# Kernel optimization log

Hardware: AMD Instinct MI355X
Metric: run time of the kernel (lower is better)

## Reference

```python
import jax, jax.numpy as jnp
import numpy as np

N = 8192
IN_DIM = 512
MEM_DIM = 512


def _linear_params(k, fan_in, fan_out):
    kw, kb = jax.random.split(k)
    s = 1.0 / np.sqrt(fan_in)
    W = jax.random.uniform(kw, (fan_in, fan_out), jnp.float32, -s, s)
    b = jax.random.uniform(kb, (fan_out,), jnp.float32, -s, s)
    return W, b


def setup_inputs() -> dict:
    key = jax.random.key(0)
    ks = jax.random.split(key, 12)
    inputs = jax.random.normal(ks[0], (N, IN_DIM), jnp.float32)
    # tree.type is a [1,2] mixing matrix per node (lang vs vis weights)
    type_mask = jax.nn.softmax(jax.random.normal(ks[1], (N, 2), jnp.float32), axis=-1)
    # topologically ordered tree: parent slot of node i is in [0, i]; slot 0 = virtual zero root state
    rng = np.random.default_rng(0)
    parent = np.zeros(N, dtype=np.int32)
    for i in range(1, N):
        parent[i] = rng.integers(0, i + 1)
    d = {"inputs": inputs, "type_mask": type_mask, "parent": jnp.asarray(parent)}
    names = ["ioux_vis", "iouh_vis", "fx_vis", "fh_vis",
             "ioux_lang", "iouh_lang", "fx_lang", "fh_lang"]
    fanins = [IN_DIM, MEM_DIM, IN_DIM, MEM_DIM] * 2
    fanouts = [3 * MEM_DIM, 3 * MEM_DIM, MEM_DIM, MEM_DIM] * 2
    for j, nm in enumerate(names):
        W, b = _linear_params(ks[2 + j], fanins[j], fanouts[j])
        d["W_" + nm] = W
        d["b_" + nm] = b
    return d


def reference(inputs, type_mask, parent,
              W_ioux_vis, b_ioux_vis, W_iouh_vis, b_iouh_vis,
              W_fx_vis, b_fx_vis, W_fh_vis, b_fh_vis,
              W_ioux_lang, b_ioux_lang, W_iouh_lang, b_iouh_lang,
              W_fx_lang, b_fx_lang, W_fh_lang, b_fh_lang):
    n_nodes = inputs.shape[0]
    D = W_fh_vis.shape[1]
    # batch the input-dependent projections into big GEMMs (fused across all nodes)
    x_iou_v = inputs @ W_ioux_vis + b_ioux_vis  # [N, 3D]
    x_f_v = inputs @ W_fx_vis + b_fx_vis        # [N, D]
    x_iou_l = inputs @ W_ioux_lang + b_ioux_lang
    x_f_l = inputs @ W_fx_lang + b_fx_lang

    def node(x_iou, x_f, h_p, c_p, W_iouh, b_iouh, W_fh, b_fh):
        iou = x_iou + h_p @ W_iouh + b_iouh  # [3D]
        i, o, u = jnp.split(iou, 3)
        f = jax.nn.sigmoid(x_f + h_p @ W_fh + b_fh)
        c = jax.nn.sigmoid(i) * jnp.tanh(u) + f * c_p
        h = jax.nn.sigmoid(o) * jnp.tanh(c)
        return c, h

    # slot 0 holds the zero state used by root nodes; node i lives at slot i+1
    c0 = jnp.zeros((n_nodes + 1, D), inputs.dtype)
    h0 = jnp.zeros((n_nodes + 1, D), inputs.dtype)

    def step(carry, xs):
        c_all, h_all = carry
        n, p, xiv, xfv, xil, xfl, tm = xs
        h_p = h_all[p]
        c_p = c_all[p]
        c_v, h_v = node(xiv, xfv, h_p, c_p, W_iouh_vis, b_iouh_vis, W_fh_vis, b_fh_vis)
        c_l, h_l = node(xil, xfl, h_p, c_p, W_iouh_lang, b_iouh_lang, W_fh_lang, b_fh_lang)
        # type_mask @ cat([lang, vis]) == tm[0]*lang + tm[1]*vis
        c_n = tm[0] * c_l + tm[1] * c_v
        h_n = tm[0] * h_l + tm[1] * h_v  # dropout is identity in eval
        return (c_all.at[n + 1].set(c_n), h_all.at[n + 1].set(h_n)), None

    idx = jnp.arange(n_nodes)
    (c_all, h_all), _ = jax.lax.scan(
        step, (c0, h0), (idx, parent, x_iou_v, x_f_v, x_iou_l, x_f_l, type_mask))
    return c_all[1:], h_all[1:]
```

## Files before the change

kernel.cpp:

```cpp
#include <hip/hip_runtime.h>
#include <math.h>

typedef unsigned short ushort_t;
typedef unsigned int uint_t;
typedef unsigned long long u64_t;
typedef __attribute__((ext_vector_type(8))) short short8;
typedef __attribute__((ext_vector_type(4))) float f32x4;

#define N_NODES 8192
#define DIM 512
#define KTOT 1024
#define NCOLS 4096
#define BM 128
#define BN 128
#define NTILE (NCOLS / BN)
#define KIT (KTOT / 32)
#define WIMG_USHORTS ((size_t)NTILE * KIT * 4096)
#define MAXLEV_LDS 128

__device__ __forceinline__ float sigm(float x) { return 1.0f / (1.0f + __expf(-x)); }
__device__ __forceinline__ float tanh_fast(float x) {
    float ax = fabsf(x);
    float e = __expf(2.0f * ax);
    float t = 1.0f - 2.0f / (e + 1.0f);
    return copysignf(t, x);
}
__device__ __forceinline__ uint_t packf(float f) {
    uint_t u = __float_as_uint(f);
    uint_t hi = u & 0xffff0000u;
    float r = f - __uint_as_float(hi);
    return hi | (__float_as_uint(r) >> 16);
}
__device__ __forceinline__ float unpackw(uint_t w) {
    return __uint_as_float(w & 0xffff0000u) + __uint_as_float(w << 16);
}
__device__ __forceinline__ uint_t rne16(float f) {
    uint_t u = __float_as_uint(f);
    return (u + 0x7fffu + ((u >> 16) & 1u)) >> 16;
}

__device__ __forceinline__ void fragAB_u32(const uint4 w0, const uint4 w1,
                                           short8& hi8, short8& lo8) {
    union { uint_t w[4]; short8 s; } H, L;
    uint_t u[8] = { w0.x, w0.y, w0.z, w0.w, w1.x, w1.y, w1.z, w1.w };
#pragma unroll
    for (int j = 0; j < 4; ++j) {
        H.w[j] = (u[2 * j + 1] & 0xffff0000u) | (u[2 * j] >> 16);
        L.w[j] = (u[2 * j + 1] << 16) | (u[2 * j] & 0xffffu);
    }
    hi8 = H.s; lo8 = L.s;
}

__device__ __forceinline__ void fragA_f32(const float4 f0, const float4 f1,
                                          short8& hi8, short8& lo8) {
    union { uint_t w[4]; short8 s; } H, L;
    float f[8] = { f0.x, f0.y, f0.z, f0.w, f1.x, f1.y, f1.z, f1.w };
#pragma unroll
    for (int j = 0; j < 4; ++j) {
        float a = f[2 * j], b = f[2 * j + 1];
        uint_t h0 = __float_as_uint(a) & 0xffff0000u;
        uint_t h1 = __float_as_uint(b) & 0xffff0000u;
        float r0 = a - __uint_as_float(h0);
        float r1 = b - __uint_as_float(h1);
        H.w[j] = h1 | (h0 >> 16);
        L.w[j] = (__float_as_uint(r1) & 0xffff0000u) | (__float_as_uint(r0) >> 16);
    }
    hi8 = H.s; lo8 = L.s;
}

__global__ void __launch_bounds__(256) prep_wimg_kernel(
    const float* __restrict__ Wx_iou_v, const float* __restrict__ Wh_iou_v,
    const float* __restrict__ Wx_f_v,   const float* __restrict__ Wh_f_v,
    const float* __restrict__ Wx_iou_l, const float* __restrict__ Wh_iou_l,
    const float* __restrict__ Wx_f_l,   const float* __restrict__ Wh_f_l,
    ushort_t* __restrict__ Wimg)
{
    __shared__ float T[32][132];
    int p = blockIdx.x >> 5, it = blockIdx.x & 31;
    int tid = threadIdx.x;
#pragma unroll
    for (int e = 0; e < 16; ++e) {
        int lin = e * 256 + tid;
        int dloc = lin & 15, kk = (lin >> 4) & 31, q = lin >> 9;
        int d = p * 16 + dloc;
        int qq = q & 3; bool lang = q >= 4;
        int k = it * 32 + kk;
        const float* W; int col, stride;
        if (qq < 3) { col = qq * DIM + d; stride = 3 * DIM;
            W = (k < DIM) ? (lang ? Wx_iou_l : Wx_iou_v) : (lang ? Wh_iou_l : Wh_iou_v); }
        else        { col = d; stride = DIM;
            W = (k < DIM) ? (lang ? Wx_f_l : Wx_f_v) : (lang ? Wh_f_l : Wh_f_v); }
        int kr = (k < DIM) ? k : (k - DIM);
        T[kk][dloc * 8 + q] = W[(size_t)kr * stride + col];
    }
    __syncthreads();
    size_t tilebase = (size_t)blockIdx.x * 4096;
#pragma unroll
    for (int gch = 0; gch < 2; ++gch) {
        int gi = gch * 256 + tid;
        int col = gi >> 2, gd = gi & 3;
        uint_t wds[4];
#pragma unroll
        for (int i = 0; i < 4; ++i) {
            uint_t v0 = rne16(T[gd * 8 + 2 * i][col]);
            uint_t v1 = rne16(T[gd * 8 + 2 * i + 1][col]);
            wds[i] = (v1 << 16) | v0;
        }
        *(uint4*)(Wimg + tilebase + (size_t)gi * 8) = make_uint4(wds[0], wds[1], wds[2], wds[3]);
    }
}

__global__ void prep_bias_kernel(
    const float* __restrict__ bx_iou_v, const float* __restrict__ bh_iou_v,
    const float* __restrict__ bx_f_v,   const float* __restrict__ bh_f_v,
    const float* __restrict__ bx_iou_l, const float* __restrict__ bh_iou_l,
    const float* __restrict__ bx_f_l,   const float* __restrict__ bh_f_l,
    float* __restrict__ bias)
{
    int j = blockIdx.x * blockDim.x + threadIdx.x;
    if (j >= NCOLS) return;
    int d = j >> 3, q = j & 7;
    int qq = q & 3;
    bool lang = (q & 4) != 0;
    const float* bx; const float* bh; int col;
    if (qq < 3) { col = qq * DIM + d; bx = lang ? bx_iou_l : bx_iou_v; bh = lang ? bh_iou_l : bh_iou_v; }
    else        { col = d;            bx = lang ? bx_f_l  : bx_f_v;   bh = lang ? bh_f_l  : bh_f_v; }
    bias[j] = bx[col] + bh[col];
}

__global__ void __launch_bounds__(1024) levels_sort_kernel(
    const int* __restrict__ parent,
    int* __restrict__ order, int* __restrict__ offsets,
    int* __restrict__ counts, int* __restrict__ cursors,
    int* __restrict__ nlev, int* __restrict__ tilestart,
    int* __restrict__ rbStart, int* __restrict__ nodeHrb)
{
    __shared__ int s_level[N_NODES];
    __shared__ int s_assigned;
    __shared__ int s_maxlev;
    int tid = threadIdx.x;
    int pr[8];
#pragma unroll
    for (int ii = 0; ii < 8; ++ii) {
        int i = tid + ii * 1024;
        pr[ii] = parent[i];
        s_level[i] = -1;
    }
    for (int i = tid; i <= N_NODES; i += 1024) counts[i] = 0;
    if (tid == 0) { s_assigned = 0; s_maxlev = 0; }
    __syncthreads();

    for (int pass = 0; pass <= N_NODES; ++pass) {
        int newly = 0;
#pragma unroll
        for (int ii = 0; ii < 8; ++ii) {
            int i = tid + ii * 1024;
            if (s_level[i] < 0) {
                int p = pr[ii];
                if (p == 0) { s_level[i] = 0; newly++; }
                else { int lp = s_level[p - 1]; if (lp >= 0) { s_level[i] = lp + 1; newly++; } }
            }
        }
        if (newly) atomicAdd(&s_assigned, newly);
        __syncthreads();
        int a = s_assigned;
        if (a >= N_NODES) break;
        __syncthreads();
    }

#pragma unroll
    for (int ii = 0; ii < 8; ++ii) {
        int i = tid + ii * 1024;
        int lv = s_level[i];
        atomicAdd(&counts[lv], 1);
        atomicMax(&s_maxlev, lv);
    }
    __syncthreads();
    if (tid == 0) {
        int nl = s_maxlev + 1;
        nlev[0] = nl;
        int off = 0, toff = 0, rb = 0;
        for (int l = 0; l < nl; ++l) {
            offsets[l] = off; cursors[l] = off;
            tilestart[l] = toff; rbStart[l] = rb;
            int mt = (counts[l] + BM - 1) / BM;
            rb += mt;
            toff += mt * NTILE;
            off += counts[l];
        }
        offsets[nl] = off;
        tilestart[nl] = toff;
        rbStart[nl] = rb;
        nlev[1] = toff;
    }
    __syncthreads();
#pragma unroll
    for (int ii = 0; ii < 8; ++ii) {
        int i = tid + ii * 1024;
        int lv = s_level[i];
        int pos = atomicAdd(&cursors[lv], 1);
        order[pos] = i;
        nodeHrb[i] = rbStart[lv] + ((pos - offsets[lv]) >> 7);
    }
}

__global__ void __launch_bounds__(256, 2) tree_fused_kernel(
    const float* __restrict__ inputs, const float* __restrict__ type_mask,
    const ushort_t* __restrict__ Wimg, const float* __restrict__ bias,
    const int* __restrict__ order, const int* __restrict__ offsets,
    const int* __restrict__ nlev, const int* __restrict__ parent,
    const int* __restrict__ rbStart,
    int* __restrict__ colCnt,
    uint_t* __restrict__ hPack, uint_t* __restrict__ cPack,
    float* __restrict__ out)
{
    float* cOut = out;
    float* hOut = out + (size_t)N_NODES * DIM;

    __shared__ float eps[BM * 132];
    __shared__ int s_node[BM];
    __shared__ int s_par[BM];
    __shared__ float s_tm[BM][2];
    __shared__ int s_rbs[MAXLEV_LDS];
    __shared__ int s_off[MAXLEV_LDS];
    __shared__ int s_cok[32];
    __shared__ int s_ok[8];

    int tid = threadIdx.x;
    int lane = tid & 63, w = tid >> 6, wr = w >> 1, wc = w & 1;
    int l15 = lane & 15, g = lane >> 4;
    int nl = nlev[0];
    int total = nlev[1];

    int nload = nl + 1; if (nload > MAXLEV_LDS) nload = MAXLEV_LDS;
    for (int i = tid; i < nload; i += 256) { s_rbs[i] = rbStart[i]; s_off[i] = offsets[i]; }
    __syncthreads();

    const ushort_t* bLane = Wimg + (size_t)(wc * 64 + l15) * 32 + (size_t)g * 8;

#define LDB(RB, tilebase, itt) { \
    _Pragma("unroll") for (int n_ = 0; n_ < 4; ++n_) \
        RB[n_] = *(const uint4*)(bLane + (size_t)(tilebase + (itt)) * 4096 + n_ * 512); }

#define LDA_H(RA, itrel) { \
    _Pragma("unroll") for (int m_ = 0; m_ < 4; ++m_) { \
        const uint4* p_ = (const uint4*)(aBaseH[m_] + (itrel) * 32 + g * 8); \
        RA[m_][0] = p_[0]; RA[m_][1] = p_[1]; } }

#define LDA_X(RA, itt) { \
    _Pragma("unroll") for (int m_ = 0; m_ < 4; ++m_) { \
        const float4* p_ = (const float4*)(aBaseX[m_] + (itt) * 32 + g * 8); \
        RA[m_][0] = p_[0]; RA[m_][1] = p_[1]; } }

#define COMP_H(RA, RB) { \
    short8 bh_[4]; \
    _Pragma("unroll") for (int n_ = 0; n_ < 4; ++n_) { \
        union { uint4 u; short8 s; } c_; c_.u = RB[n_]; bh_[n_] = c_.s; } \
    _Pragma("unroll") for (int m_ = 0; m_ < 4; ++m_) { \
        short8 ah_, al_; fragAB_u32(RA[m_][0], RA[m_][1], ah_, al_); \
        _Pragma("unroll") for (int n_ = 0; n_ < 4; ++n_) { \
            acc[m_][n_] = __builtin_amdgcn_mfma_f32_16x16x32_bf16(ah_, bh_[n_], acc[m_][n_], 0, 0, 0); \
            acc[m_][n_] = __builtin_amdgcn_mfma_f32_16x16x32_bf16(al_, bh_[n_], acc[m_][n_], 0, 0, 0); } } }

#define COMP_X(RA, RB) { \
    short8 bh_[4]; \
    _Pragma("unroll") for (int n_ = 0; n_ < 4; ++n_) { \
        union { uint4 u; short8 s; } c_; c_.u = RB[n_]; bh_[n_] = c_.s; } \
    _Pragma("unroll") for (int m_ = 0; m_ < 4; ++m_) { \
        short8 ah_, al_; fragA_f32(RA[m_][0], RA[m_][1], ah_, al_); \
        _Pragma("unroll") for (int n_ = 0; n_ < 4; ++n_) { \
            acc[m_][n_] = __builtin_amdgcn_mfma_f32_16x16x32_bf16(ah_, bh_[n_], acc[m_][n_], 0, 0, 0); \
            acc[m_][n_] = __builtin_amdgcn_mfma_f32_16x16x32_bf16(al_, bh_[n_], acc[m_][n_], 0, 0, 0); } } }

#define WAIT_GROUPS(colPrev, nPrev, gq) { \
    for (;;) { \
        if (tid < 32) \
            s_cok[tid] = (__hip_atomic_load(&(colPrev)[tid], __ATOMIC_RELAXED, \
                                            __HIP_MEMORY_SCOPE_AGENT) >= (nPrev)) ? 1 : 0; \
        __syncthreads(); \
        if (tid < 8) { \
            if (s_cok[4 * tid] && s_cok[4 * tid + 1] && s_cok[4 * tid + 2] && s_cok[4 * tid + 3]) \
                s_ok[tid] = 1; \
        } \
        __syncthreads(); \
        if (s_ok[gq]) break; \
        __builtin_amdgcn_s_sleep(4); \
    } }

    for (int t = blockIdx.x; t < total; t += gridDim.x) {
        int lev = 0;
        while (lev + 1 < nload && s_rbs[lev + 1] * NTILE <= t) ++lev;
        int lt = t - s_rbs[lev] * NTILE;
        int ntile = lt % NTILE;
        int mt = lt / NTILE;
        int start = s_off[lev];
        int cnt = s_off[lev + 1] - start;
        int jc = ntile * BN;
        int r0 = mt * BM;
        int tbx = ntile * KIT;
        int tbh = ntile * KIT + 16;

        if (tid < BM) {
            int r = r0 + tid;
            int node = (r < cnt) ? order[start + r] : -1;
            s_node[tid] = node;
            int p = (node >= 0) ? parent[node] : 0;
            s_par[tid] = p;
            float t0 = 0.f, t1 = 0.f;
            if (node >= 0) { t0 = type_mask[node * 2]; t1 = type_mask[node * 2 + 1]; }
            s_tm[tid][0] = t0; s_tm[tid][1] = t1;
        }
        if (tid < 32) s_cok[tid] = 0;
        if (tid < 8) s_ok[tid] = 0;
        __syncthreads();

        f32x4 acc[4][4];
#pragma unroll
        for (int m = 0; m < 4; ++m)
#pragma unroll
            for (int n = 0; n < 4; ++n) acc[m][n] = (f32x4)(0.f);

        {
            const float* aBaseX[4];
#pragma unroll
            for (int m = 0; m < 4; ++m) {
                int nd = s_node[wr * 64 + m * 16 + l15];
                aBaseX[m] = inputs + (size_t)(nd < 0 ? 0 : nd) * DIM;
            }
            float4 xa0[4][2], xa1[4][2]; uint4 xb0[4], xb1[4];
            LDA_X(xa0, 0); LDB(xb0, tbx, 0);
#pragma unroll
            for (int ii = 0; ii < 8; ++ii) {
                int e = 2 * ii, o = e + 1;
                LDA_X(xa1, o); LDB(xb1, tbx, o);
                __builtin_amdgcn_s_setprio(1);
                COMP_X(xa0, xb0);
                __builtin_amdgcn_s_setprio(0);
                if (e + 2 < 16) { LDA_X(xa0, e + 2); LDB(xb0, tbx, e + 2); }
                __builtin_amdgcn_s_setprio(1);
                COMP_X(xa1, xb1);
                __builtin_amdgcn_s_setprio(0);
            }
        }

        if (lev > 0) {
            const int* colPrev = colCnt + (lev - 1) * NTILE;
            int nPrev = s_rbs[lev] - s_rbs[lev - 1];
            const int gb = ntile >> 2;

            const uint_t* aBaseH[4];
#pragma unroll
            for (int m = 0; m < 4; ++m) {
                int p = s_par[wr * 64 + m * 16 + l15];
                aBaseH[m] = hPack + (size_t)((p > 0) ? (p - 1) : 0) * DIM;
            }

            uint4 ha0[4][2], ha1[4][2]; uint4 hb0[4], hb1[4];
            WAIT_GROUPS(colPrev, nPrev, gb);
            LDA_H(ha0, 2 * gb); LDB(hb0, tbh, 2 * gb);
            LDA_H(ha1, 2 * gb + 1); LDB(hb1, tbh, 2 * gb + 1);
#pragma unroll
            for (int s = 0; s < 8; ++s) {
                const int gn = (gb + s + 1) & 7;
                __builtin_amdgcn_s_setprio(1);
                COMP_H(ha0, hb0);
                __builtin_amdgcn_s_setprio(0);
                if (s < 7) {
                    if (!s_ok[gn]) WAIT_GROUPS(colPrev, nPrev, gn);
                    LDA_H(ha0, 2 * gn); LDB(hb0, tbh, 2 * gn);
                }
                __builtin_amdgcn_s_setprio(1);
                COMP_H(ha1, hb1);
                __builtin_amdgcn_s_setprio(0);
                if (s < 7) { LDA_H(ha1, 2 * gn + 1); LDB(hb1, tbh, 2 * gn + 1); }
            }
        }

        int cntloc = cnt - r0; if (cntloc > BM) cntloc = BM;

        float CP[8];
#pragma unroll
        for (int e = 0; e < 8; ++e) {
            int task = e * 256 + tid;
            int row = task >> 4, dl = task & 15;
            CP[e] = 0.f;
            if (row < cntloc) {
                int p = s_par[row];
                if (p > 0) {
                    int d = (jc + dl * 8) >> 3;
                    CP[e] = unpackw(cPack[(size_t)(p - 1) * DIM + d]);
                }
            }
        }

#pragma unroll
        for (int m = 0; m < 4; ++m)
#pragma unroll
            for (int n = 0; n < 4; ++n) {
                int row = wr * 64 + m * 16 + g * 4;
                int c = wc * 64 + n * 16 + l15;
#pragma unroll
                for (int r = 0; r < 4; ++r) eps[(row + r) * 132 + c] = acc[m][n][r];
            }
        __syncthreads();

        float CN[8], HN[8];
#pragma unroll
        for (int e = 0; e < 8; ++e) {
            int task = e * 256 + tid;
            int row = task >> 4, dl = task & 15;
            CN[e] = 0.f; HN[e] = 0.f;
            if (row < cntloc) {
                int node = s_node[row];
                const float* ep = &eps[row * 132 + dl * 8];
                float4 v0 = *(const float4*)ep;
                float4 v1 = *(const float4*)(ep + 4);
                int jb = jc + dl * 8;
                float4 b0 = *(const float4*)(bias + jb);
                float4 b1 = *(const float4*)(bias + jb + 4);
                float cp = CP[e];
                float cv = sigm(v0.x + b0.x) * tanh_fast(v0.z + b0.z)
                         + sigm(v0.w + b0.w) * cp;
                float hv = sigm(v0.y + b0.y) * tanh_fast(cv);
                float cl = sigm(v1.x + b1.x) * tanh_fast(v1.z + b1.z)
                         + sigm(v1.w + b1.w) * cp;
                float hl = sigm(v1.y + b1.y) * tanh_fast(cl);
                float tm0 = s_tm[row][0], tm1 = s_tm[row][1];
                float cn = tm0 * cl + tm1 * cv;
                float hn2 = tm0 * hl + tm1 * hv;
                CN[e] = cn; HN[e] = hn2;
                size_t oi = (size_t)node * DIM + (jb >> 3);
                __hip_atomic_store(&cPack[oi], packf(cn),
                                   __ATOMIC_RELAXED, __HIP_MEMORY_SCOPE_AGENT);
                __hip_atomic_store(&hPack[oi], packf(hn2),
                                   __ATOMIC_RELAXED, __HIP_MEMORY_SCOPE_AGENT);
            }
        }

        __builtin_amdgcn_s_waitcnt(0);
        __syncthreads();
        if (tid == 0)
            __hip_atomic_fetch_add(&colCnt[lev * NTILE + ntile], 1,
                                   __ATOMIC_RELAXED, __HIP_MEMORY_SCOPE_AGENT);

#pragma unroll
        for (int e = 0; e < 8; ++e) {
            int task = e * 256 + tid;
            int row = task >> 4, dl = task & 15;
            if (row < cntloc) {
                int node = s_node[row];
                size_t oi = (size_t)node * DIM + ((jc + dl * 8) >> 3);
                cOut[oi] = CN[e];
                hOut[oi] = HN[e];
            }
        }
        __syncthreads();
    }
#undef LDB
#undef LDA_H
#undef LDA_X
#undef COMP_H
#undef COMP_X
#undef WAIT_GROUPS
}

extern "C" void kernel_launch(void* const* d_in, const int* in_sizes, int n_in,
                              void* d_out, int out_size, void* d_ws, size_t ws_size,
                              hipStream_t stream) {
    const float* inputs      = (const float*)d_in[0];
    const float* type_mask   = (const float*)d_in[1];
    const int*   parent      = (const int*)d_in[2];
    const float* W_ioux_vis  = (const float*)d_in[3];
    const float* b_ioux_vis  = (const float*)d_in[4];
    const float* W_iouh_vis  = (const float*)d_in[5];
    const float* b_iouh_vis  = (const float*)d_in[6];
    const float* W_fx_vis    = (const float*)d_in[7];
    const float* b_fx_vis    = (const float*)d_in[8];
    const float* W_fh_vis    = (const float*)d_in[9];
    const float* b_fh_vis    = (const float*)d_in[10];
    const float* W_ioux_lang = (const float*)d_in[11];
    const float* b_ioux_lang = (const float*)d_in[12];
    const float* W_iouh_lang = (const float*)d_in[13];
    const float* b_iouh_lang = (const float*)d_in[14];
    const float* W_fx_lang   = (const float*)d_in[15];
    const float* b_fx_lang   = (const float*)d_in[16];
    const float* W_fh_lang   = (const float*)d_in[17];
    const float* b_fh_lang   = (const float*)d_in[18];

    ushort_t* Wimg = (ushort_t*)d_ws;
    float* bias    = (float*)(Wimg + WIMG_USHORTS);
    int* order     = (int*)(bias + NCOLS);
    int* offsets   = order + N_NODES;
    int* counts    = offsets + (N_NODES + 2);
    int* cursors   = counts + (N_NODES + 2);
    int* nlev      = cursors + (N_NODES + 2);
    int* tilestart = nlev + 8;
    int* rbStart   = tilestart + (N_NODES + 2);
    int* nodeHrb   = rbStart + (N_NODES + 2);
    int* colCnt    = nodeHrb + N_NODES;
    size_t off2 = (size_t)((char*)(colCnt + MAXLEV_LDS * NTILE) - (char*)d_ws);
    off2 = (off2 + 255) & ~(size_t)255;
    uint_t* hPack = (uint_t*)((char*)d_ws + off2);
    uint_t* cPack = hPack + (size_t)N_NODES * DIM;

    float* out = (float*)d_out;

    hipMemsetAsync((void*)colCnt, 0, MAXLEV_LDS * NTILE * sizeof(int), stream);

    hipLaunchKernelGGL(prep_wimg_kernel, dim3(NTILE * KIT), dim3(256), 0, stream,
                       W_ioux_vis, W_iouh_vis, W_fx_vis, W_fh_vis,
                       W_ioux_lang, W_iouh_lang, W_fx_lang, W_fh_lang, Wimg);
    hipLaunchKernelGGL(prep_bias_kernel, dim3(NCOLS / 256), dim3(256), 0, stream,
                       b_ioux_vis, b_iouh_vis, b_fx_vis, b_fh_vis,
                       b_ioux_lang, b_iouh_lang, b_fx_lang, b_fh_lang, bias);
    hipLaunchKernelGGL(levels_sort_kernel, dim3(1), dim3(1024), 0, stream,
                       parent, order, offsets, counts, cursors, nlev, tilestart,
                       rbStart, nodeHrb);

    int occ = 0;
    if (hipOccupancyMaxActiveBlocksPerMultiprocessor(&occ, (const void*)tree_fused_kernel, 256, 0) != hipSuccess || occ < 1)
        occ = 1;
    int bpc = occ < 2 ? occ : 2;
    dim3 grid(256 * bpc);

    void* args[] = { (void*)&inputs, (void*)&type_mask, (void*)&Wimg, (void*)&bias,
                     (void*)&order, (void*)&offsets, (void*)&nlev, (void*)&parent,
                     (void*)&rbStart, (void*)&colCnt,
                     (void*)&hPack, (void*)&cPack, (void*)&out };
    hipLaunchCooperativeKernel((const void*)tree_fused_kernel, grid, dim3(256), args, 0, stream);
}
```

Before: 807.8 us.

## Split tree tile across eight waves and gate dependency waits per wave

Doubles the block to 512 threads so each of eight waves computes 32 rows of the 128x128 tile instead of 64, halving per-wave accumulators and A-fragment loads. Replaces the block-wide dependency wait, which used shared flags and two __syncthreads per poll, with a per-wave gate that polls the four column counters itself and tracks satisfied groups in a register mask. It also moves the odd-step prefetch to the end of the loop body. The aim is more latency hiding and less barrier cost on the critical recurrence path. In exchange, the register budget per thread is tighter under the new launch bounds, and more waves poll global counters at once.

```diff
diff --git a/kernel.cpp b/kernel.cpp
--- a/kernel.cpp
+++ b/kernel.cpp
@@ -204,7 +204,7 @@
     }
 }
 
-__global__ void __launch_bounds__(256, 2) tree_fused_kernel(
+__global__ void __launch_bounds__(512, 2) tree_fused_kernel(
     const float* __restrict__ inputs, const float* __restrict__ type_mask,
     const ushort_t* __restrict__ Wimg, const float* __restrict__ bias,
     const int* __restrict__ order, const int* __restrict__ offsets,
@@ -223,17 +223,16 @@
     __shared__ float s_tm[BM][2];
     __shared__ int s_rbs[MAXLEV_LDS];
     __shared__ int s_off[MAXLEV_LDS];
-    __shared__ int s_cok[32];
-    __shared__ int s_ok[8];
 
     int tid = threadIdx.x;
-    int lane = tid & 63, w = tid >> 6, wr = w >> 1, wc = w & 1;
+    int lane = tid & 63, w = tid >> 6;
+    int wr = w >> 1, wc = w & 1;
     int l15 = lane & 15, g = lane >> 4;
     int nl = nlev[0];
     int total = nlev[1];
 
     int nload = nl + 1; if (nload > MAXLEV_LDS) nload = MAXLEV_LDS;
-    for (int i = tid; i < nload; i += 256) { s_rbs[i] = rbStart[i]; s_off[i] = offsets[i]; }
+    for (int i = tid; i < nload; i += 512) { s_rbs[i] = rbStart[i]; s_off[i] = offsets[i]; }
     __syncthreads();
 
     const ushort_t* bLane = Wimg + (size_t)(wc * 64 + l15) * 32 + (size_t)g * 8;
@@ -243,12 +242,12 @@
         RB[n_] = *(const uint4*)(bLane + (size_t)(tilebase + (itt)) * 4096 + n_ * 512); }
 
 #define LDA_H(RA, itrel) { \
-    _Pragma("unroll") for (int m_ = 0; m_ < 4; ++m_) { \
+    _Pragma("unroll") for (int m_ = 0; m_ < 2; ++m_) { \
         const uint4* p_ = (const uint4*)(aBaseH[m_] + (itrel) * 32 + g * 8); \
         RA[m_][0] = p_[0]; RA[m_][1] = p_[1]; } }
 
 #define LDA_X(RA, itt) { \
-    _Pragma("unroll") for (int m_ = 0; m_ < 4; ++m_) { \
+    _Pragma("unroll") for (int m_ = 0; m_ < 2; ++m_) { \
         const float4* p_ = (const float4*)(aBaseX[m_] + (itt) * 32 + g * 8); \
         RA[m_][0] = p_[0]; RA[m_][1] = p_[1]; } }
 
@@ -256,7 +255,7 @@
     short8 bh_[4]; \
     _Pragma("unroll") for (int n_ = 0; n_ < 4; ++n_) { \
         union { uint4 u; short8 s; } c_; c_.u = RB[n_]; bh_[n_] = c_.s; } \
-    _Pragma("unroll") for (int m_ = 0; m_ < 4; ++m_) { \
+    _Pragma("unroll") for (int m_ = 0; m_ < 2; ++m_) { \
         short8 ah_, al_; fragAB_u32(RA[m_][0], RA[m_][1], ah_, al_); \
         _Pragma("unroll") for (int n_ = 0; n_ < 4; ++n_) { \
             acc[m_][n_] = __builtin_amdgcn_mfma_f32_16x16x32_bf16(ah_, bh_[n_], acc[m_][n_], 0, 0, 0); \
@@ -266,25 +265,26 @@
     short8 bh_[4]; \
     _Pragma("unroll") for (int n_ = 0; n_ < 4; ++n_) { \
         union { uint4 u; short8 s; } c_; c_.u = RB[n_]; bh_[n_] = c_.s; } \
-    _Pragma("unroll") for (int m_ = 0; m_ < 4; ++m_) { \
+    _Pragma("unroll") for (int m_ = 0; m_ < 2; ++m_) { \
         short8 ah_, al_; fragA_f32(RA[m_][0], RA[m_][1], ah_, al_); \
         _Pragma("unroll") for (int n_ = 0; n_ < 4; ++n_) { \
             acc[m_][n_] = __builtin_amdgcn_mfma_f32_16x16x32_bf16(ah_, bh_[n_], acc[m_][n_], 0, 0, 0); \
             acc[m_][n_] = __builtin_amdgcn_mfma_f32_16x16x32_bf16(al_, bh_[n_], acc[m_][n_], 0, 0, 0); } } }
 
-#define WAIT_GROUPS(colPrev, nPrev, gq) { \
-    for (;;) { \
-        if (tid < 32) \
-            s_cok[tid] = (__hip_atomic_load(&(colPrev)[tid], __ATOMIC_RELAXED, \
-                                            __HIP_MEMORY_SCOPE_AGENT) >= (nPrev)) ? 1 : 0; \
-        __syncthreads(); \
-        if (tid < 8) { \
-            if (s_cok[4 * tid] && s_cok[4 * tid + 1] && s_cok[4 * tid + 2] && s_cok[4 * tid + 3]) \
-                s_ok[tid] = 1; \
+#define WAVE_GATE(colPrev, nPrev, gq, slp) { \
+    if (!(gmask & (1 << (gq)))) { \
+        for (;;) { \
+            int okv = 1; \
+            if (lane < 4) { \
+                int c_ = __hip_atomic_load(&(colPrev)[4 * (gq) + lane], __ATOMIC_RELAXED, \
+                                           __HIP_MEMORY_SCOPE_AGENT); \
+                okv = (c_ >= (nPrev)) ? 1 : 0; \
+            } \
+            if (__all(okv)) break; \
+            __builtin_amdgcn_s_sleep(slp); \
         } \
-        __syncthreads(); \
-        if (s_ok[gq]) break; \
-        __builtin_amdgcn_s_sleep(4); \
+        gmask |= (1 << (gq)); \
+        asm volatile("" ::: "memory"); \
     } }
 
     for (int t = blockIdx.x; t < total; t += gridDim.x) {
@@ -310,29 +310,27 @@
             if (node >= 0) { t0 = type_mask[node * 2]; t1 = type_mask[node * 2 + 1]; }
             s_tm[tid][0] = t0; s_tm[tid][1] = t1;
         }
-        if (tid < 32) s_cok[tid] = 0;
-        if (tid < 8) s_ok[tid] = 0;
         __syncthreads();
 
-        f32x4 acc[4][4];
-#pragma unroll
-        for (int m = 0; m < 4; ++m)
+        f32x4 acc[2][4];
+#pragma unroll
+        for (int m = 0; m < 2; ++m)
 #pragma unroll
             for (int n = 0; n < 4; ++n) acc[m][n] = (f32x4)(0.f);
 
         {
-            const float* aBaseX[4];
-#pragma unroll
-            for (int m = 0; m < 4; ++m) {
-                int nd = s_node[wr * 64 + m * 16 + l15];
+            const float* aBaseX[2];
+#pragma unroll
+            for (int m = 0; m < 2; ++m) {
+                int nd = s_node[wr * 32 + m * 16 + l15];
                 aBaseX[m] = inputs + (size_t)(nd < 0 ? 0 : nd) * DIM;
             }
-            float4 xa0[4][2], xa1[4][2]; uint4 xb0[4], xb1[4];
+            float4 xa0[2][2], xa1[2][2]; uint4 xb0[4], xb1[4];
             LDA_X(xa0, 0); LDB(xb0, tbx, 0);
+            LDA_X(xa1, 1); LDB(xb1, tbx, 1);
 #pragma unroll
             for (int ii = 0; ii < 8; ++ii) {
                 int e = 2 * ii, o = e + 1;
-                LDA_X(xa1, o); LDB(xb1, tbx, o);
                 __builtin_amdgcn_s_setprio(1);
                 COMP_X(xa0, xb0);
                 __builtin_amdgcn_s_setprio(0);
@@ -340,6 +338,7 @@
                 __builtin_amdgcn_s_setprio(1);
                 COMP_X(xa1, xb1);
                 __builtin_amdgcn_s_setprio(0);
+                if (o + 2 < 16) { LDA_X(xa1, o + 2); LDB(xb1, tbx, o + 2); }
             }
         }
 
@@ -347,16 +346,17 @@
             const int* colPrev = colCnt + (lev - 1) * NTILE;
             int nPrev = s_rbs[lev] - s_rbs[lev - 1];
             const int gb = ntile >> 2;
-
-            const uint_t* aBaseH[4];
-#pragma unroll
-            for (int m = 0; m < 4; ++m) {
-                int p = s_par[wr * 64 + m * 16 + l15];
+            uint_t gmask = 0;
+
+            const uint_t* aBaseH[2];
+#pragma unroll
+            for (int m = 0; m < 2; ++m) {
+                int p = s_par[wr * 32 + m * 16 + l15];
                 aBaseH[m] = hPack + (size_t)((p > 0) ? (p - 1) : 0) * DIM;
             }
 
-            uint4 ha0[4][2], ha1[4][2]; uint4 hb0[4], hb1[4];
-            WAIT_GROUPS(colPrev, nPrev, gb);
+            uint4 ha0[2][2], ha1[2][2]; uint4 hb0[4], hb1[4];
+            WAVE_GATE(colPrev, nPrev, gb, 4);
             LDA_H(ha0, 2 * gb); LDB(hb0, tbh, 2 * gb);
             LDA_H(ha1, 2 * gb + 1); LDB(hb1, tbh, 2 * gb + 1);
 #pragma unroll
@@ -366,7 +366,7 @@
                 COMP_H(ha0, hb0);
                 __builtin_amdgcn_s_setprio(0);
                 if (s < 7) {
-                    if (!s_ok[gn]) WAIT_GROUPS(colPrev, nPrev, gn);
+                    WAVE_GATE(colPrev, nPrev, gn, 1);
                     LDA_H(ha0, 2 * gn); LDB(hb0, tbh, 2 * gn);
                 }
                 __builtin_amdgcn_s_setprio(1);
@@ -378,10 +378,10 @@
 
         int cntloc = cnt - r0; if (cntloc > BM) cntloc = BM;
 
-        float CP[8];
-#pragma unroll
-        for (int e = 0; e < 8; ++e) {
-            int task = e * 256 + tid;
+        float CP[4];
+#pragma unroll
+        for (int e = 0; e < 4; ++e) {
+            int task = e * 512 + tid;
             int row = task >> 4, dl = task & 15;
             CP[e] = 0.f;
             if (row < cntloc) {
@@ -394,20 +394,20 @@
         }
 
 #pragma unroll
-        for (int m = 0; m < 4; ++m)
+        for (int m = 0; m < 2; ++m)
 #pragma unroll
             for (int n = 0; n < 4; ++n) {
-                int row = wr * 64 + m * 16 + g * 4;
+                int row = wr * 32 + m * 16 + g * 4;
                 int c = wc * 64 + n * 16 + l15;
 #pragma unroll
                 for (int r = 0; r < 4; ++r) eps[(row + r) * 132 + c] = acc[m][n][r];
             }
         __syncthreads();
 
-        float CN[8], HN[8];
-#pragma unroll
-        for (int e = 0; e < 8; ++e) {
-            int task = e * 256 + tid;
+        float CN[4], HN[4];
+#pragma unroll
+        for (int e = 0; e < 4; ++e) {
+            int task = e * 512 + tid;
             int row = task >> 4, dl = task & 15;
             CN[e] = 0.f; HN[e] = 0.f;
             if (row < cntloc) {
@@ -444,8 +444,8 @@
                                    __ATOMIC_RELAXED, __HIP_MEMORY_SCOPE_AGENT);
 
 #pragma unroll
-        for (int e = 0; e < 8; ++e) {
-            int task = e * 256 + tid;
+        for (int e = 0; e < 4; ++e) {
+            int task = e * 512 + tid;
             int row = task >> 4, dl = task & 15;
             if (row < cntloc) {
                 int node = s_node[row];
@@ -461,7 +461,7 @@
 #undef LDA_X
 #undef COMP_H
 #undef COMP_X
-#undef WAIT_GROUPS
+#undef WAVE_GATE
 }
 
 extern "C" void kernel_launch(void* const* d_in, const int* in_sizes, int n_in,
@@ -518,7 +518,7 @@
                        rbStart, nodeHrb);
 
     int occ = 0;
-    if (hipOccupancyMaxActiveBlocksPerMultiprocessor(&occ, (const void*)tree_fused_kernel, 256, 0) != hipSuccess || occ < 1)
+    if (hipOccupancyMaxActiveBlocksPerMultiprocessor(&occ, (const void*)tree_fused_kernel, 512, 0) != hipSuccess || occ < 1)
         occ = 1;
     int bpc = occ < 2 ? occ : 2;
     dim3 grid(256 * bpc);
@@ -527,5 +527,5 @@
                      (void*)&order, (void*)&offsets, (void*)&nlev, (void*)&parent,
                      (void*)&rbStart, (void*)&colCnt,
                      (void*)&hPack, (void*)&cPack, (void*)&out };
-    hipLaunchCooperativeKernel((const void*)tree_fused_kernel, grid, dim3(256), args, 0, stream);
-}
+    hipLaunchCooperativeKernel((const void*)tree_fused_kernel, grid, dim3(512), args, 0, stream);
+}
```

Result: no change. 809.4 us (+0.2%).
